# Optimization experiments

Measured on AMD Instinct MI355X. Metric: run time of the kernel, lower is better.

Reference implementation:

```python
import jax, jax.numpy as jnp
import numpy as np

N_NODES = 50000
HID = 256


def _gcn_norm(edge_index, n_nodes):
    # PyG GCNConv default: add self-loops, symmetric normalization
    src, dst = edge_index[0], edge_index[1]
    loop = jnp.arange(n_nodes, dtype=src.dtype)
    src = jnp.concatenate([src, loop])
    dst = jnp.concatenate([dst, loop])
    deg = jax.ops.segment_sum(jnp.ones_like(src, dtype=jnp.float32), dst, num_segments=n_nodes)
    dinv = jnp.where(deg > 0, jax.lax.rsqrt(jnp.maximum(deg, 1.0)), 0.0)
    norm = dinv[src] * dinv[dst]  # [E + N]
    return src, dst, norm


def _gcn_conv(x, W, b, src, dst, norm, n_nodes):
    h = x @ W                                   # [N, H] dense transform first (PyG order)
    msg = h[src] * norm[:, None]                # gather + scale
    out = jax.ops.segment_sum(msg, dst, num_segments=n_nodes)
    return out + b


def setup_inputs() -> dict:
    key = jax.random.key(0)
    ks = jax.random.split(key, 8)
    x = jax.random.normal(ks[0], (N_NODES, HID), dtype=jnp.float32)
    edge_index = jax.random.randint(ks[1], (2, 1600000), 0, N_NODES, dtype=jnp.int64)
    s = 1.0 / np.sqrt(HID)
    W1 = jax.random.normal(ks[2], (HID, HID), dtype=jnp.float32) * s
    b1 = jnp.zeros((HID,), dtype=jnp.float32)
    Wmu = jax.random.normal(ks[3], (HID, HID), dtype=jnp.float32) * s
    bmu = jnp.zeros((HID,), dtype=jnp.float32)
    Wls = jax.random.normal(ks[4], (HID, HID), dtype=jnp.float32) * s * 0.1
    bls = jnp.zeros((HID,), dtype=jnp.float32)
    return {"x": x, "edge_index": edge_index, "W1": W1, "b1": b1,
            "Wmu": Wmu, "bmu": bmu, "Wls": Wls, "bls": bls}


def reference(x, edge_index, W1, b1, Wmu, bmu, Wls, bls):
    n = x.shape[0]
    src, dst, norm = _gcn_norm(edge_index, n)
    h = jax.nn.relu(_gcn_conv(x, W1, b1, src, dst, norm, n))
    mu = _gcn_conv(h, Wmu, bmu, src, dst, norm, n)
    logstd = _gcn_conv(h, Wls, bls, src, dst, norm, n)
    std = jnp.exp(logstd)
    eps = jax.random.normal(jax.random.key(1), std.shape, dtype=std.dtype)
    z = mu + std * eps
    return (z, mu, logstd)
```

## Files before the change

### kernel.cpp

```cpp
#include <hip/hip_runtime.h>
#include <stdint.h>

#define HID 256

typedef __bf16 bf16x8 __attribute__((ext_vector_type(8)));
typedef float  f32x4  __attribute__((ext_vector_type(4)));
typedef unsigned int uint4v __attribute__((ext_vector_type(4)));

__device__ __forceinline__ unsigned short f2bf(float f){
  unsigned int x = __float_as_uint(f);
  x += 0x7FFFu + ((x >> 16) & 1u);
  return (unsigned short)(x >> 16);
}
__device__ __forceinline__ float bf2f(unsigned int u){
  return __uint_as_float(u << 16);
}
__device__ __forceinline__ float bflo(unsigned int x){ return __uint_as_float(x << 16); }
__device__ __forceinline__ float bfhi(unsigned int x){ return __uint_as_float(x & 0xFFFF0000u); }
__device__ __forceinline__ bf16x8 ntload8(const unsigned short* p){
  uint4v t = __builtin_nontemporal_load((const uint4v*)p);
  return __builtin_bit_cast(bf16x8, t);
}

__global__ void count_kernel(const int* __restrict__ ei, int E, int* __restrict__ deg){
  int e = blockIdx.x*256 + threadIdx.x;
  if (e < E) atomicAdd(&deg[ei[E + e]], 1);
}

__global__ void dinv_kernel(const int* __restrict__ deg, float* __restrict__ dinv, int N){
  int i = blockIdx.x*256 + threadIdx.x;
  if (i < N) dinv[i] = 1.0f / sqrtf((float)(deg[i] + 1));
}

__global__ void scan1_kernel(const int* __restrict__ deg, int* __restrict__ rowptr,
                             int* __restrict__ partials, int N){
  __shared__ int sm[256];
  int t = threadIdx.x;
  int i = blockIdx.x*256 + t;
  int v = (i < N) ? deg[i] : 0;
  int acc = v;
  sm[t] = acc;
  __syncthreads();
  for (int off = 1; off < 256; off <<= 1){
    int add = (t >= off) ? sm[t - off] : 0;
    __syncthreads();
    acc += add;
    sm[t] = acc;
    __syncthreads();
  }
  if (i < N) rowptr[i] = acc - v;
  if (t == 255) partials[blockIdx.x] = acc;
}

__global__ void scan2_kernel(int* __restrict__ partials, int nb){
  __shared__ int sm[256];
  int t = threadIdx.x;
  int v = (t < nb) ? partials[t] : 0;
  int acc = v;
  sm[t] = acc;
  __syncthreads();
  for (int off = 1; off < 256; off <<= 1){
    int add = (t >= off) ? sm[t - off] : 0;
    __syncthreads();
    acc += add;
    sm[t] = acc;
    __syncthreads();
  }
  if (t < nb) partials[t] = acc - v;
}

__global__ void scan3_kernel(int* __restrict__ rowptr, const int* __restrict__ partials,
                             int N, int E){
  int i = blockIdx.x*256 + threadIdx.x;
  if (i < N) rowptr[i] += partials[blockIdx.x];
  if (i == 0) rowptr[N] = E;
}

__global__ void scatter_kernel(const int* __restrict__ ei, int E, const int* __restrict__ rowptr,
                               int* __restrict__ fill, const float* __restrict__ dinv,
                               int* __restrict__ col, float* __restrict__ wgt){
  int e = blockIdx.x*256 + threadIdx.x;
  if (e >= E) return;
  int s = ei[e];
  int d = ei[E + e];
  int p = rowptr[d] + atomicAdd(&fill[d], 1);
  col[p] = s;
  wgt[p] = dinv[s] * dinv[d];
}

__global__ void convX_kernel(const float* __restrict__ x, unsigned short* __restrict__ xb, int total8){
  int t = blockIdx.x*256 + threadIdx.x;
  if (t >= total8) return;
  const float* p = x + (size_t)t*8;
  f32x4 a = *(const f32x4*)p;
  f32x4 b = *(const f32x4*)(p + 4);
  ushort4 o0, o1;
  o0.x = f2bf(a[0]); o0.y = f2bf(a[1]); o0.z = f2bf(a[2]); o0.w = f2bf(a[3]);
  o1.x = f2bf(b[0]); o1.y = f2bf(b[1]); o1.z = f2bf(b[2]); o1.w = f2bf(b[3]);
  ushort4* q = (ushort4*)(xb + (size_t)t*8);
  q[0] = o0; q[1] = o1;
}

__global__ void convW_kernel(const float* __restrict__ W1, const float* __restrict__ Wmu,
                             const float* __restrict__ Wls, unsigned short* __restrict__ Wt){
  int t = blockIdx.x*256 + threadIdx.x;
  if (t >= 3*65536) return;
  int m = t >> 16;
  int r = t & 0xFFFF;
  int n = r >> 8, k = r & 255;
  int ksrc = (m == 0) ? k : ((k & ~63) | ((k & 3) << 4) | ((k >> 2) & 15));
  const float* W = (m == 0) ? W1 : (m == 1 ? Wmu : Wls);
  Wt[t] = f2bf(W[ksrc*HID + n]);
}

__global__ void agg_bf16(const unsigned short* __restrict__ X, unsigned short* __restrict__ Y,
                         const int* __restrict__ rowptr, const int* __restrict__ col,
                         const float* __restrict__ wgt, const float* __restrict__ dinv,
                         int N, int sin, int sout){
  int w = (blockIdx.x * blockDim.x + threadIdx.x) >> 6;
  int lane = threadIdx.x & 63;
  if (w >= N) return;
  int q  = lane >> 4;
  int cl = lane & 15;
  float acc[16];
  #pragma unroll
  for (int k = 0; k < 16; ++k) acc[k] = 0.f;
  int p0 = rowptr[w], p1 = rowptr[w+1];
  for (int base = p0; base < p1; base += 64){
    int idx = base + lane;
    int sc = 0; float wc = 0.f;
    if (idx < p1){ sc = col[idx]; wc = wgt[idx]; }
    int cnt = min(p1 - base, 64);
    for (int j = 0; j < cnt; j += 4){
      int   s = __shfl(sc, j + q);
      float f = __shfl(wc, j + q);
      const unsigned short* rp = X + (size_t)s*sin + cl*16;
      uint4v u0 = *(const uint4v*)rp;
      uint4v u1 = *(const uint4v*)(rp + 8);
      acc[ 0]=fmaf(bflo(u0.x),f,acc[ 0]); acc[ 1]=fmaf(bfhi(u0.x),f,acc[ 1]);
      acc[ 2]=fmaf(bflo(u0.y),f,acc[ 2]); acc[ 3]=fmaf(bfhi(u0.y),f,acc[ 3]);
      acc[ 4]=fmaf(bflo(u0.z),f,acc[ 4]); acc[ 5]=fmaf(bfhi(u0.z),f,acc[ 5]);
      acc[ 6]=fmaf(bflo(u0.w),f,acc[ 6]); acc[ 7]=fmaf(bfhi(u0.w),f,acc[ 7]);
      acc[ 8]=fmaf(bflo(u1.x),f,acc[ 8]); acc[ 9]=fmaf(bfhi(u1.x),f,acc[ 9]);
      acc[10]=fmaf(bflo(u1.y),f,acc[10]); acc[11]=fmaf(bfhi(u1.y),f,acc[11]);
      acc[12]=fmaf(bflo(u1.z),f,acc[12]); acc[13]=fmaf(bfhi(u1.z),f,acc[13]);
      acc[14]=fmaf(bflo(u1.w),f,acc[14]); acc[15]=fmaf(bfhi(u1.w),f,acc[15]);
    }
  }
  #pragma unroll
  for (int k = 0; k < 16; ++k){
    acc[k] += __shfl_xor(acc[k], 16);
    acc[k] += __shfl_xor(acc[k], 32);
  }
  if (q == 0){
    float s2 = dinv[w]; s2 *= s2;
    const unsigned short* rp = X + (size_t)w*sin + cl*16;
    uint4v u0 = *(const uint4v*)rp;
    uint4v u1 = *(const uint4v*)(rp + 8);
    acc[ 0]=fmaf(bflo(u0.x),s2,acc[ 0]); acc[ 1]=fmaf(bfhi(u0.x),s2,acc[ 1]);
    acc[ 2]=fmaf(bflo(u0.y),s2,acc[ 2]); acc[ 3]=fmaf(bfhi(u0.y),s2,acc[ 3]);
    acc[ 4]=fmaf(bflo(u0.z),s2,acc[ 4]); acc[ 5]=fmaf(bfhi(u0.z),s2,acc[ 5]);
    acc[ 6]=fmaf(bflo(u0.w),s2,acc[ 6]); acc[ 7]=fmaf(bfhi(u0.w),s2,acc[ 7]);
    acc[ 8]=fmaf(bflo(u1.x),s2,acc[ 8]); acc[ 9]=fmaf(bfhi(u1.x),s2,acc[ 9]);
    acc[10]=fmaf(bflo(u1.y),s2,acc[10]); acc[11]=fmaf(bfhi(u1.y),s2,acc[11]);
    acc[12]=fmaf(bflo(u1.z),s2,acc[12]); acc[13]=fmaf(bfhi(u1.z),s2,acc[13]);
    acc[14]=fmaf(bflo(u1.w),s2,acc[14]); acc[15]=fmaf(bfhi(u1.w),s2,acc[15]);
    uint4v o0, o1;
    o0.x = (unsigned int)f2bf(acc[ 0]) | ((unsigned int)f2bf(acc[ 1]) << 16);
    o0.y = (unsigned int)f2bf(acc[ 2]) | ((unsigned int)f2bf(acc[ 3]) << 16);
    o0.z = (unsigned int)f2bf(acc[ 4]) | ((unsigned int)f2bf(acc[ 5]) << 16);
    o0.w = (unsigned int)f2bf(acc[ 6]) | ((unsigned int)f2bf(acc[ 7]) << 16);
    o1.x = (unsigned int)f2bf(acc[ 8]) | ((unsigned int)f2bf(acc[ 9]) << 16);
    o1.y = (unsigned int)f2bf(acc[10]) | ((unsigned int)f2bf(acc[11]) << 16);
    o1.z = (unsigned int)f2bf(acc[12]) | ((unsigned int)f2bf(acc[13]) << 16);
    o1.w = (unsigned int)f2bf(acc[14]) | ((unsigned int)f2bf(acc[15]) << 16);
    uint4v* yp = (uint4v*)(Y + (size_t)w*sout + cl*16);
    yp[0] = o0; yp[1] = o1;
  }
}

__global__ __launch_bounds__(256, 8) void gemm1_kernel(const unsigned short* __restrict__ A,
    const unsigned short* __restrict__ Bt, const float* __restrict__ bias,
    unsigned short* __restrict__ H, int N){
  int r0 = blockIdx.x * 32;
  int lane = threadIdx.x & 63;
  int nw = threadIdx.x >> 6;
  int lr = lane & 15, kg = lane >> 4;
  f32x4 acc[2][4] = {};
  for (int ks = 0; ks < 8; ++ks){
    int kb = ks*32 + kg*8;
    bf16x8 af[2];
    #pragma unroll
    for (int rf = 0; rf < 2; ++rf){
      int row = r0 + rf*16 + lr; if (row > N-1) row = N-1;
      af[rf] = *(const bf16x8*)(A + (size_t)row*HID + kb);
    }
    #pragma unroll
    for (int cf = 0; cf < 4; ++cf){
      int c = nw*64 + cf*16 + lr;
      bf16x8 bfr = *(const bf16x8*)(Bt + (size_t)c*HID + kb);
      acc[0][cf] = __builtin_amdgcn_mfma_f32_16x16x32_bf16(af[0], bfr, acc[0][cf], 0, 0, 0);
      acc[1][cf] = __builtin_amdgcn_mfma_f32_16x16x32_bf16(af[1], bfr, acc[1][cf], 0, 0, 0);
    }
  }
  float bv[4];
  #pragma unroll
  for (int cf = 0; cf < 4; ++cf) bv[cf] = bias[nw*64 + cf*16 + lr];
  #pragma unroll
  for (int rf = 0; rf < 2; ++rf){
    #pragma unroll
    for (int i = 0; i < 4; ++i){
      int row = r0 + rf*16 + kg*4 + i;
      if (row < N){
        ushort4 o;
        o.x = f2bf(fmaxf(acc[rf][0][i] + bv[0], 0.0f));
        o.y = f2bf(fmaxf(acc[rf][1][i] + bv[1], 0.0f));
        o.z = f2bf(fmaxf(acc[rf][2][i] + bv[2], 0.0f));
        o.w = f2bf(fmaxf(acc[rf][3][i] + bv[3], 0.0f));
        *(ushort4*)(H + (size_t)row*HID + nw*64 + lr*4) = o;
      }
    }
  }
}

__device__ __forceinline__ unsigned int rotl32(unsigned int v, int r){
  return (v << r) | (v >> (32 - r));
}

__device__ __forceinline__ float gauss_eps(unsigned int idxv){
  unsigned int x0 = 0u, x1 = idxv;
  const unsigned int ks0 = 0u, ks1 = 1u, ks2 = 0x1BD11BDAu ^ 0u ^ 1u;
  x0 += ks0; x1 += ks1;
#define TFR(r) { x0 += x1; x1 = rotl32(x1, r); x1 ^= x0; }
  TFR(13) TFR(15) TFR(26) TFR(6)   x0 += ks1; x1 += ks2 + 1u;
  TFR(17) TFR(29) TFR(16) TFR(24)  x0 += ks2; x1 += ks0 + 2u;
  TFR(13) TFR(15) TFR(26) TFR(6)   x0 += ks0; x1 += ks1 + 3u;
  TFR(17) TFR(29) TFR(16) TFR(24)  x0 += ks1; x1 += ks2 + 4u;
  TFR(13) TFR(15) TFR(26) TFR(6)   x0 += ks2; x1 += ks0 + 5u;
#undef TFR
  unsigned int bits = x0 ^ x1;
  float f = __uint_as_float((bits >> 9) | 0x3F800000u) - 1.0f;
  const float lo = -0.99999994f;
  float u = fmaxf(lo, fmaf(f, 2.0f, lo));
  float t = fmaf(-u, u, 1.0f);
  float wv = -0.69314718056f * __builtin_amdgcn_logf(t);
  float p;
  if (wv < 5.0f){
    wv -= 2.5f;
    p = 2.81022636e-08f;
    p = fmaf(p, wv, 3.43273939e-07f);
    p = fmaf(p, wv, -3.5233877e-06f);
    p = fmaf(p, wv, -4.39150654e-06f);
    p = fmaf(p, wv, 0.00021858087f);
    p = fmaf(p, wv, -0.00125372503f);
    p = fmaf(p, wv, -0.00417768164f);
    p = fmaf(p, wv, 0.246640727f);
    p = fmaf(p, wv, 1.50140941f);
  } else {
    wv = sqrtf(wv) - 3.0f;
    p = -0.000200214257f;
    p = fmaf(p, wv, 0.000100950558f);
    p = fmaf(p, wv, 0.00134934322f);
    p = fmaf(p, wv, -0.00367342844f);
    p = fmaf(p, wv, 0.00573950773f);
    p = fmaf(p, wv, -0.0076224613f);
    p = fmaf(p, wv, 0.00943887047f);
    p = fmaf(p, wv, 1.00167406f);
    p = fmaf(p, wv, 2.83297682f);
  }
  return 1.4142135381698608f * (p * u);
}

__global__ __launch_bounds__(256, 5) void gemm2_kernel(const unsigned short* __restrict__ A2b,
    const unsigned short* __restrict__ Bt, const float* __restrict__ bias,
    float* __restrict__ OUT, int N, int sa){
  __shared__ float sml[16][260];
  int r0 = blockIdx.x * 32;
  int lane = threadIdx.x & 63;
  int nw = threadIdx.x >> 6;
  int lr = lane & 15, kg = lane >> 4;
  f32x4 acc[2][4] = {};
  for (int ks = 0; ks < 8; ++ks){
    int kb = ks*32 + kg*8;
    bf16x8 af[2];
    #pragma unroll
    for (int rf = 0; rf < 2; ++rf){
      int row = r0 + rf*16 + lr; if (row > N-1) row = N-1;
      af[rf] = ntload8(A2b + (size_t)row*sa + kb);
    }
    #pragma unroll
    for (int cf = 0; cf < 4; ++cf){
      int c = nw*64 + cf*16 + lr;
      bf16x8 bfr = *(const bf16x8*)(Bt + (size_t)c*HID + kb);
      acc[0][cf] = __builtin_amdgcn_mfma_f32_16x16x32_bf16(af[0], bfr, acc[0][cf], 0, 0, 0);
      acc[1][cf] = __builtin_amdgcn_mfma_f32_16x16x32_bf16(af[1], bfr, acc[1][cf], 0, 0, 0);
    }
  }
  f32x4 b4 = *(const f32x4*)(bias + lane*4);
  for (int rf = 0; rf < 2; ++rf){
    #pragma unroll
    for (int cf = 0; cf < 4; ++cf){
      int c = nw*64 + cf*16 + lr;
      #pragma unroll
      for (int i = 0; i < 4; ++i) sml[kg*4 + i][c] = acc[rf][cf][i];
    }
    __syncthreads();
    #pragma unroll
    for (int rr = 0; rr < 4; ++rr){
      int rl = nw*4 + rr;
      int row = r0 + rf*16 + rl;
      if (row < N){
        f32x4 m4 = *(const f32x4*)&sml[rl][lane*4];
        m4 += b4;
        __builtin_nontemporal_store(m4, (f32x4*)(OUT + (size_t)row*HID + lane*4));
      }
    }
    __syncthreads();
  }
}

__global__ __launch_bounds__(256, 5) void gemm3_kernel(const unsigned short* __restrict__ A2b,
    const unsigned short* __restrict__ Bt, const float* __restrict__ bias,
    const float* __restrict__ MU, float* __restrict__ Z, float* __restrict__ LS, int N, int sa){
  __shared__ float sml[16][260];
  int r0 = blockIdx.x * 32;
  int lane = threadIdx.x & 63;
  int nw = threadIdx.x >> 6;
  int lr = lane & 15, kg = lane >> 4;
  f32x4 acc[2][4] = {};
  for (int ks = 0; ks < 8; ++ks){
    int kb = ks*32 + kg*8;
    bf16x8 af[2];
    #pragma unroll
    for (int rf = 0; rf < 2; ++rf){
      int row = r0 + rf*16 + lr; if (row > N-1) row = N-1;
      af[rf] = ntload8(A2b + (size_t)row*sa + kb);
    }
    #pragma unroll
    for (int cf = 0; cf < 4; ++cf){
      int c = nw*64 + cf*16 + lr;
      bf16x8 bfr = *(const bf16x8*)(Bt + (size_t)c*HID + kb);
      acc[0][cf] = __builtin_amdgcn_mfma_f32_16x16x32_bf16(af[0], bfr, acc[0][cf], 0, 0, 0);
      acc[1][cf] = __builtin_amdgcn_mfma_f32_16x16x32_bf16(af[1], bfr, acc[1][cf], 0, 0, 0);
    }
  }
  f32x4 b4 = *(const f32x4*)(bias + lane*4);
  for (int rf = 0; rf < 2; ++rf){
    #pragma unroll
    for (int cf = 0; cf < 4; ++cf){
      int c = nw*64 + cf*16 + lr;
      #pragma unroll
      for (int i = 0; i < 4; ++i) sml[kg*4 + i][c] = acc[rf][cf][i];
    }
    __syncthreads();
    #pragma unroll
    for (int rr = 0; rr < 4; ++rr){
      int rl = nw*4 + rr;
      int row = r0 + rf*16 + rl;
      if (row < N){
        size_t base = (size_t)row*HID + lane*4;
        f32x4 l4 = *(const f32x4*)&sml[rl][lane*4];
        l4 += b4;
        f32x4 m4 = *(const f32x4*)(MU + base);
        f32x4 z4;
        #pragma unroll
        for (int j = 0; j < 4; ++j){
          float e = gauss_eps((unsigned int)(base + j));
          float s = __builtin_amdgcn_exp2f(l4[j] * 1.44269504f);
          z4[j] = fmaf(s, e, m4[j]);
        }
        __builtin_nontemporal_store(z4, (f32x4*)(Z  + base));
        __builtin_nontemporal_store(l4, (f32x4*)(LS + base));
      }
    }
    __syncthreads();
  }
}

extern "C" void kernel_launch(void* const* d_in, const int* in_sizes, int n_in,
                              void* d_out, int out_size, void* d_ws, size_t ws_size,
                              hipStream_t stream){
  const float* x   = (const float*)d_in[0];
  const int*   ei  = (const int*)d_in[1];
  const float* W1  = (const float*)d_in[2];
  const float* b1  = (const float*)d_in[3];
  const float* Wmu = (const float*)d_in[4];
  const float* bmu = (const float*)d_in[5];
  const float* Wls = (const float*)d_in[6];
  const float* bls = (const float*)d_in[7];
  const int N = in_sizes[0] / HID;
  const int E = in_sizes[1] / 2;
  const size_t NA = ((size_t)N + 64) & ~(size_t)63;

  int* deg      = (int*)d_ws;
  int* fill     = deg + NA;
  int* rowptr   = fill + NA;
  int* partials = rowptr + NA;
  float* dinv   = (float*)(partials + 1024);
  int*  col     = (int*)(dinv + NA);
  float* wgt    = (float*)(col + (size_t)E);
  unsigned short* Wt = (unsigned short*)(wgt + (size_t)E);
  unsigned short* a2ws = Wt + 3*65536;

  float* Z  = (float*)d_out;
  float* MU = Z + (size_t)N*HID;
  float* LS = MU + (size_t)N*HID;
  unsigned short* hb  = (unsigned short*)Z;
  unsigned short* xb  = (unsigned short*)Z + (size_t)N*HID;
  unsigned short* a1b = (unsigned short*)MU;

  size_t ws_used = (size_t)((char*)a2ws - (char*)d_ws);
  bool packed = (ws_size >= ws_used + (size_t)N * 256 * sizeof(unsigned short));
  unsigned short* a2b = packed ? a2ws : (unsigned short*)LS;
  int sa = packed ? 256 : 512;

  hipMemsetAsync(deg, 0, NA*2*sizeof(int), stream);

  int ebl = (E + 255)/256, nbl = (N + 255)/256;
  count_kernel  <<<ebl, 256, 0, stream>>>(ei, E, deg);
  dinv_kernel   <<<nbl, 256, 0, stream>>>(deg, dinv, N);
  scan1_kernel  <<<nbl, 256, 0, stream>>>(deg, rowptr, partials, N);
  scan2_kernel  <<<1,   256, 0, stream>>>(partials, nbl);
  scan3_kernel  <<<nbl, 256, 0, stream>>>(rowptr, partials, N, E);
  scatter_kernel<<<ebl, 256, 0, stream>>>(ei, E, rowptr, fill, dinv, col, wgt);
  convW_kernel  <<<768, 256, 0, stream>>>(W1, Wmu, Wls, Wt);
  convX_kernel  <<<(N*HID/8 + 255)/256, 256, 0, stream>>>(x, xb, N*HID/8);

  agg_bf16    <<<(N + 3)/4,  256, 0, stream>>>(xb, a1b, rowptr, col, wgt, dinv, N, 256, 256);
  gemm1_kernel<<<(N + 31)/32, 256, 0, stream>>>(a1b, Wt, b1, hb, N);
  agg_bf16    <<<(N + 3)/4,  256, 0, stream>>>(hb, a2b, rowptr, col, wgt, dinv, N, 256, sa);
  gemm2_kernel<<<(N + 31)/32, 256, 0, stream>>>(a2b, Wt + 65536,   bmu, MU, N, sa);
  gemm3_kernel<<<(N + 31)/32, 256, 0, stream>>>(a2b, Wt + 2*65536, bls, MU, Z, LS, N, sa);
}
```

Before: 761.7 us.

## Split aggregation into column slices, pack edge col/weight, slice-major GEMM input

Aggregation now runs as eight column-slice blocks per group of nodes, each gathering 64 bytes per neighbour row. Blocks working on the same slice touch a smaller feature working set, which is meant to improve L2 hit rates on the random gathers. The output is written slice-major, and the GEMM kernels' A loads are adjusted to read that layout. Column index and edge weight are packed into one int2 array to halve index loads, and nontemporal loads are dropped. The cost is 8x more blocks, each re-reading the edge list and rowptr for its node.

```diff
diff --git a/kernel.cpp b/kernel.cpp
--- a/kernel.cpp
+++ b/kernel.cpp
@@ -12,15 +12,8 @@
   x += 0x7FFFu + ((x >> 16) & 1u);
   return (unsigned short)(x >> 16);
 }
-__device__ __forceinline__ float bf2f(unsigned int u){
-  return __uint_as_float(u << 16);
-}
 __device__ __forceinline__ float bflo(unsigned int x){ return __uint_as_float(x << 16); }
 __device__ __forceinline__ float bfhi(unsigned int x){ return __uint_as_float(x & 0xFFFF0000u); }
-__device__ __forceinline__ bf16x8 ntload8(const unsigned short* p){
-  uint4v t = __builtin_nontemporal_load((const uint4v*)p);
-  return __builtin_bit_cast(bf16x8, t);
-}
 
 __global__ void count_kernel(const int* __restrict__ ei, int E, int* __restrict__ deg){
   int e = blockIdx.x*256 + threadIdx.x;
@@ -78,14 +71,14 @@
 
 __global__ void scatter_kernel(const int* __restrict__ ei, int E, const int* __restrict__ rowptr,
                                int* __restrict__ fill, const float* __restrict__ dinv,
-                               int* __restrict__ col, float* __restrict__ wgt){
+                               int2* __restrict__ ew){
   int e = blockIdx.x*256 + threadIdx.x;
   if (e >= E) return;
   int s = ei[e];
   int d = ei[E + e];
   int p = rowptr[d] + atomicAdd(&fill[d], 1);
-  col[p] = s;
-  wgt[p] = dinv[s] * dinv[d];
+  int2 v; v.x = s; v.y = __float_as_int(dinv[s] * dinv[d]);
+  ew[p] = v;
 }
 
 __global__ void convX_kernel(const float* __restrict__ x, unsigned short* __restrict__ xb, int total8){
@@ -97,8 +90,8 @@
   ushort4 o0, o1;
   o0.x = f2bf(a[0]); o0.y = f2bf(a[1]); o0.z = f2bf(a[2]); o0.w = f2bf(a[3]);
   o1.x = f2bf(b[0]); o1.y = f2bf(b[1]); o1.z = f2bf(b[2]); o1.w = f2bf(b[3]);
-  ushort4* q = (ushort4*)(xb + (size_t)t*8);
-  q[0] = o0; q[1] = o1;
+  ushort4* qq = (ushort4*)(xb + (size_t)t*8);
+  qq[0] = o0; qq[1] = o1;
 }
 
 __global__ void convW_kernel(const float* __restrict__ W1, const float* __restrict__ Wmu,
@@ -113,10 +106,52 @@
   Wt[t] = f2bf(W[ksrc*HID + n]);
 }
 
-__global__ void agg_bf16(const unsigned short* __restrict__ X, unsigned short* __restrict__ Y,
-                         const int* __restrict__ rowptr, const int* __restrict__ col,
-                         const float* __restrict__ wgt, const float* __restrict__ dinv,
-                         int N, int sin, int sout){
+__global__ void agg_slice(const unsigned short* __restrict__ X, unsigned short* __restrict__ Y,
+                          const int* __restrict__ rowptr, const int2* __restrict__ ew,
+                          const float* __restrict__ dinv, int N, int sin){
+  int slice = blockIdx.x & 7;
+  int w = ((blockIdx.x >> 3) << 2) + (threadIdx.x >> 6);
+  if (w >= N) return;
+  int lane = threadIdx.x & 63;
+  int q = lane >> 4, cl = lane & 15;
+  const unsigned short* Xs = X + slice*32 + cl*2;
+  float a0 = 0.f, a1 = 0.f;
+  int p0 = rowptr[w], p1 = rowptr[w+1];
+  for (int base = p0; base < p1; base += 64){
+    int idx = base + lane;
+    int sc = 0; float wc = 0.f;
+    if (idx < p1){ int2 e = ew[idx]; sc = e.x; wc = __int_as_float(e.y); }
+    int cnt = min(p1 - base, 64);
+    int j = 0;
+    for (; j + 8 <= cnt; j += 8){
+      int   s0 = __shfl(sc, j + q),     s1 = __shfl(sc, j + 4 + q);
+      float f0 = __shfl(wc, j + q),     f1 = __shfl(wc, j + 4 + q);
+      unsigned int u0 = *(const unsigned int*)(Xs + (size_t)s0*sin);
+      unsigned int u1 = *(const unsigned int*)(Xs + (size_t)s1*sin);
+      a0 = fmaf(bflo(u0), f0, a0); a1 = fmaf(bfhi(u0), f0, a1);
+      a0 = fmaf(bflo(u1), f1, a0); a1 = fmaf(bfhi(u1), f1, a1);
+    }
+    for (; j < cnt; j += 4){
+      int   s = __shfl(sc, j + q);
+      float f = __shfl(wc, j + q);
+      unsigned int u = *(const unsigned int*)(Xs + (size_t)s*sin);
+      a0 = fmaf(bflo(u), f, a0); a1 = fmaf(bfhi(u), f, a1);
+    }
+  }
+  a0 += __shfl_xor(a0, 16); a1 += __shfl_xor(a1, 16);
+  a0 += __shfl_xor(a0, 32); a1 += __shfl_xor(a1, 32);
+  if (q == 0){
+    float s2 = dinv[w]; s2 *= s2;
+    unsigned int u = *(const unsigned int*)(Xs + (size_t)w*sin);
+    a0 = fmaf(bflo(u), s2, a0); a1 = fmaf(bfhi(u), s2, a1);
+    unsigned int o = (unsigned int)f2bf(a0) | ((unsigned int)f2bf(a1) << 16);
+    *(unsigned int*)(Y + (size_t)slice*N*32 + (size_t)w*32 + cl*2) = o;
+  }
+}
+
+__global__ void agg_full(const unsigned short* __restrict__ X, unsigned short* __restrict__ Y,
+                         const int* __restrict__ rowptr, const int2* __restrict__ ew,
+                         const float* __restrict__ dinv, int N, int sin, int sout){
   int w = (blockIdx.x * blockDim.x + threadIdx.x) >> 6;
   int lane = threadIdx.x & 63;
   if (w >= N) return;
@@ -129,7 +164,7 @@
   for (int base = p0; base < p1; base += 64){
     int idx = base + lane;
     int sc = 0; float wc = 0.f;
-    if (idx < p1){ sc = col[idx]; wc = wgt[idx]; }
+    if (idx < p1){ int2 e = ew[idx]; sc = e.x; wc = __int_as_float(e.y); }
     int cnt = min(p1 - base, 64);
     for (int j = 0; j < cnt; j += 4){
       int   s = __shfl(sc, j + q);
@@ -186,6 +221,7 @@
   int lane = threadIdx.x & 63;
   int nw = threadIdx.x >> 6;
   int lr = lane & 15, kg = lane >> 4;
+  size_t sl = (size_t)N * 32;
   f32x4 acc[2][4] = {};
   for (int ks = 0; ks < 8; ++ks){
     int kb = ks*32 + kg*8;
@@ -193,7 +229,7 @@
     #pragma unroll
     for (int rf = 0; rf < 2; ++rf){
       int row = r0 + rf*16 + lr; if (row > N-1) row = N-1;
-      af[rf] = *(const bf16x8*)(A + (size_t)row*HID + kb);
+      af[rf] = *(const bf16x8*)(A + (size_t)ks*sl + (size_t)row*32 + kg*8);
     }
     #pragma unroll
     for (int cf = 0; cf < 4; ++cf){
@@ -273,12 +309,13 @@
 
 __global__ __launch_bounds__(256, 5) void gemm2_kernel(const unsigned short* __restrict__ A2b,
     const unsigned short* __restrict__ Bt, const float* __restrict__ bias,
-    float* __restrict__ OUT, int N, int sa){
+    float* __restrict__ OUT, int N, int sa, int sliced){
   __shared__ float sml[16][260];
   int r0 = blockIdx.x * 32;
   int lane = threadIdx.x & 63;
   int nw = threadIdx.x >> 6;
   int lr = lane & 15, kg = lane >> 4;
+  size_t sl = (size_t)N * 32;
   f32x4 acc[2][4] = {};
   for (int ks = 0; ks < 8; ++ks){
     int kb = ks*32 + kg*8;
@@ -286,7 +323,9 @@
     #pragma unroll
     for (int rf = 0; rf < 2; ++rf){
       int row = r0 + rf*16 + lr; if (row > N-1) row = N-1;
-      af[rf] = ntload8(A2b + (size_t)row*sa + kb);
+      size_t aoff = sliced ? ((size_t)ks*sl + (size_t)row*32 + kg*8)
+                           : ((size_t)row*sa + kb);
+      af[rf] = *(const bf16x8*)(A2b + aoff);
     }
     #pragma unroll
     for (int cf = 0; cf < 4; ++cf){
@@ -321,12 +360,14 @@
 
 __global__ __launch_bounds__(256, 5) void gemm3_kernel(const unsigned short* __restrict__ A2b,
     const unsigned short* __restrict__ Bt, const float* __restrict__ bias,
-    const float* __restrict__ MU, float* __restrict__ Z, float* __restrict__ LS, int N, int sa){
+    const float* __restrict__ MU, float* __restrict__ Z, float* __restrict__ LS,
+    int N, int sa, int sliced){
   __shared__ float sml[16][260];
   int r0 = blockIdx.x * 32;
   int lane = threadIdx.x & 63;
   int nw = threadIdx.x >> 6;
   int lr = lane & 15, kg = lane >> 4;
+  size_t sl = (size_t)N * 32;
   f32x4 acc[2][4] = {};
   for (int ks = 0; ks < 8; ++ks){
     int kb = ks*32 + kg*8;
@@ -334,7 +375,9 @@
     #pragma unroll
     for (int rf = 0; rf < 2; ++rf){
       int row = r0 + rf*16 + lr; if (row > N-1) row = N-1;
-      af[rf] = ntload8(A2b + (size_t)row*sa + kb);
+      size_t aoff = sliced ? ((size_t)ks*sl + (size_t)row*32 + kg*8)
+                           : ((size_t)row*sa + kb);
+      af[rf] = *(const bf16x8*)(A2b + aoff);
     }
     #pragma unroll
     for (int cf = 0; cf < 4; ++cf){
@@ -397,9 +440,8 @@
   int* rowptr   = fill + NA;
   int* partials = rowptr + NA;
   float* dinv   = (float*)(partials + 1024);
-  int*  col     = (int*)(dinv + NA);
-  float* wgt    = (float*)(col + (size_t)E);
-  unsigned short* Wt = (unsigned short*)(wgt + (size_t)E);
+  int2* ew      = (int2*)(dinv + NA);
+  unsigned short* Wt = (unsigned short*)(ew + (size_t)E);
   unsigned short* a2ws = Wt + 3*65536;
 
   float* Z  = (float*)d_out;
@@ -413,6 +455,7 @@
   bool packed = (ws_size >= ws_used + (size_t)N * 256 * sizeof(unsigned short));
   unsigned short* a2b = packed ? a2ws : (unsigned short*)LS;
   int sa = packed ? 256 : 512;
+  int sliced2 = packed ? 1 : 0;
 
   hipMemsetAsync(deg, 0, NA*2*sizeof(int), stream);
 
@@ -422,13 +465,18 @@
   scan1_kernel  <<<nbl, 256, 0, stream>>>(deg, rowptr, partials, N);
   scan2_kernel  <<<1,   256, 0, stream>>>(partials, nbl);
   scan3_kernel  <<<nbl, 256, 0, stream>>>(rowptr, partials, N, E);
-  scatter_kernel<<<ebl, 256, 0, stream>>>(ei, E, rowptr, fill, dinv, col, wgt);
+  scatter_kernel<<<ebl, 256, 0, stream>>>(ei, E, rowptr, fill, dinv, ew);
   convW_kernel  <<<768, 256, 0, stream>>>(W1, Wmu, Wls, Wt);
   convX_kernel  <<<(N*HID/8 + 255)/256, 256, 0, stream>>>(x, xb, N*HID/8);
 
-  agg_bf16    <<<(N + 3)/4,  256, 0, stream>>>(xb, a1b, rowptr, col, wgt, dinv, N, 256, 256);
+  int abl = ((N + 3)/4) * 8;
+  agg_slice   <<<abl, 256, 0, stream>>>(xb, a1b, rowptr, ew, dinv, N, 256);
   gemm1_kernel<<<(N + 31)/32, 256, 0, stream>>>(a1b, Wt, b1, hb, N);
-  agg_bf16    <<<(N + 3)/4,  256, 0, stream>>>(hb, a2b, rowptr, col, wgt, dinv, N, 256, sa);
-  gemm2_kernel<<<(N + 31)/32, 256, 0, stream>>>(a2b, Wt + 65536,   bmu, MU, N, sa);
-  gemm3_kernel<<<(N + 31)/32, 256, 0, stream>>>(a2b, Wt + 2*65536, bls, MU, Z, LS, N, sa);
-}
+  if (packed){
+    agg_slice <<<abl, 256, 0, stream>>>(hb, a2b, rowptr, ew, dinv, N, 256);
+  } else {
+    agg_full  <<<(N + 3)/4, 256, 0, stream>>>(hb, a2b, rowptr, ew, dinv, N, 256, sa);
+  }
+  gemm2_kernel<<<(N + 31)/32, 256, 0, stream>>>(a2b, Wt + 65536,   bmu, MU, N, sa, sliced2);
+  gemm3_kernel<<<(N + 31)/32, 256, 0, stream>>>(a2b, Wt + 2*65536, bls, MU, Z, LS, N, sa, sliced2);
+}
```

Measured after the change: 884.1 us. +16.1%, slower.
